# Kernel tuning notes

Measured on AMD Instinct MI355X. Metric: run time of the kernel, lower is better.

The kernel has to match this reference:

```python
import jax, jax.numpy as jnp
import numpy as np

L1, L2, L3, COUNT, B = 3072, 15, 32, 8, 16384

def setup_inputs() -> dict:
    key = jax.random.key(0)
    ks = jax.random.split(key, 10)
    s = 1.0 / np.sqrt(L1)
    inp = {
        'x': jax.random.normal(ks[0], (B, L1), dtype=jnp.float32),
        'ls_indices': jax.random.randint(ks[1], (B,), 0, COUNT, dtype=jnp.int64 if jax.config.jax_enable_x64 else jnp.int32),
        # l1: Linear(L1, (L2+1)*count)
        'l1_w': jax.random.uniform(ks[2], ((L2 + 1) * COUNT, L1), jnp.float32, -s, s),
        'l1_b': jax.random.uniform(ks[3], ((L2 + 1) * COUNT,), jnp.float32, -s, s),
        # l1_fact: Linear(L1, L2+1) -- zero-initialized in the original module
        'l1f_w': jnp.zeros((L2 + 1, L1), jnp.float32),
        'l1f_b': jnp.zeros((L2 + 1,), jnp.float32),
        # l2: Linear(2*L2, L3*count)
        'l2_w': jax.random.uniform(ks[4], (L3 * COUNT, 2 * L2), jnp.float32, -0.18, 0.18),
        'l2_b': jax.random.uniform(ks[5], (L3 * COUNT,), jnp.float32, -0.18, 0.18),
        # output: Linear(L3, count) -- bias zero-initialized
        'out_w': jax.random.uniform(ks[6], (COUNT, L3), jnp.float32, -0.176, 0.176),
        'out_b': jnp.zeros((COUNT,), jnp.float32),
    }
    return inp

def reference(x, ls_indices, l1_w, l1_b, l1f_w, l1f_b, l2_w, l2_b, out_w, out_b):
    Bn = x.shape[0]
    rows = jnp.arange(Bn)
    idx = ls_indices.astype(jnp.int32)

    # l1: compute all stacks, gather selected
    l1s = (x @ l1_w.T + l1_b).reshape(Bn, COUNT, L2 + 1)   # [B, count, 16]
    l1c = l1s[rows, idx]                                    # [B, 16]
    l1f = x @ l1f_w.T + l1f_b                               # [B, 16]
    l1c_main, l1c_out = l1c[:, :L2], l1c[:, L2:]            # [B,15],[B,1]
    l1f_main, l1f_out = l1f[:, :L2], l1f[:, L2:]

    l1x = l1c_main + l1f_main                               # [B, 15]
    l1x = jnp.clip(jnp.concatenate([jnp.square(l1x) * (127.0 / 128.0), l1x], axis=1), 0.0, 1.0)  # [B, 30]

    # l2
    l2s = (l1x @ l2_w.T + l2_b).reshape(Bn, COUNT, L3)      # [B, count, 32]
    l2x = jnp.clip(l2s[rows, idx], 0.0, 1.0)                # [B, 32]

    # output
    l3s = l2x @ out_w.T + out_b                             # [B, count]
    l3c = l3s[rows, idx][:, None]                           # [B, 1]
    return l3c + l1f_out + l1c_out                          # [B, 1]
```

## Files before the change

kernel.cpp:

```cpp
#include <hip/hip_runtime.h>
#include <hip/hip_bf16.h>

#define BATCH 16384
#define K1DIM 3072
#define NCOUNT 8
#define NO 16
#define CHUNK 256
#define NCHUNK (K1DIM / CHUNK)

typedef float f32x4 __attribute__((ext_vector_type(4)));
typedef unsigned int u32;

__host__ __device__ constexpr int brev5(int i) {
    int r = 0;
    for (int b = 0; b < 5; ++b) r |= ((i >> b) & 1) << (4 - b);
    return r;
}

__global__ __launch_bounds__(256) void k_combine(const float* __restrict__ l1w,
                                                 const float* __restrict__ l1fw,
                                                 float* __restrict__ wc) {
    int i = blockIdx.x * 256 + threadIdx.x;
    int row = i / 768;
    int col = (i - row * 768) * 4;
    int o = row & 15;
    f32x4 a = *(const f32x4*)(l1w + (size_t)row * K1DIM + col);
    f32x4 f = *(const f32x4*)(l1fw + (size_t)o * K1DIM + col);
    *(f32x4*)(wc + (size_t)row * K1DIM + col) = a + f;
}

__global__ __launch_bounds__(256) void k_bucket(const int* __restrict__ ls,
                                                int* __restrict__ counts,
                                                int* __restrict__ bucketArr) {
    __shared__ int h[NCOUNT];
    __shared__ int hbase[NCOUNT];
    int t = threadIdx.x;
    if (t < NCOUNT) h[t] = 0;
    __syncthreads();
    int i = blockIdx.x * 256 + t;
    int idx = ls[i];
    int lpos = atomicAdd(&h[idx], 1);
    __syncthreads();
    if (t < NCOUNT) hbase[t] = atomicAdd(&counts[t], h[t]);
    __syncthreads();
    bucketArr[idx * BATCH + hbase[idx] + lpos] = i;
}

__device__ __forceinline__ void stage4(const float* gbase, float* lds_linear,
                                       int wid, int lane) {
#pragma unroll
    for (int i = 0; i < 4; ++i) {
        int row = wid * 4 + i;
        const float* g = gbase + (size_t)row * K1DIM + lane * 4;
        float* l = lds_linear + row * CHUNK;
        __builtin_amdgcn_global_load_lds(
            (const __attribute__((address_space(1))) u32*)g,
            (__attribute__((address_space(3))) u32*)l, 16, 0, 0);
    }
}

__global__ __launch_bounds__(256, 5) void k_gemm(
    const float* __restrict__ x, const float* __restrict__ wc_all,
    const float* __restrict__ l1b, const float* __restrict__ l1fb,
    const int* __restrict__ bucketArr, const int* __restrict__ counts,
    float* __restrict__ y) {
    __shared__ float buf[2][NO * CHUNK];

    int cnt[NCOUNT], off[NCOUNT];
    int nblk = 0;
#pragma unroll
    for (int i = 0; i < NCOUNT; ++i) {
        cnt[i] = counts[i];
        off[i] = nblk;
        nblk += (cnt[i] + 7) >> 3;
    }
    int b = blockIdx.x;
    if (b >= nblk) return;
    int bucket = 0;
#pragma unroll
    for (int i = 1; i < NCOUNT; ++i) if (b >= off[i]) bucket = i;
    int chunkblk = b - off[bucket];
    int count = cnt[bucket];

    int t = threadIdx.x;
    int lane = t & 63;
    int wid = t >> 6;

    const int* bk = bucketArr + bucket * BATCH;
    int base = chunkblk * 8 + wid * 2;
    int g0 = min(base + 0, count - 1);
    int g1 = min(base + 1, count - 1);
    int sid0 = bk[g0], sid1 = bk[g1];
    const float* xr0 = x + (size_t)sid0 * K1DIM + lane * 4;
    const float* xr1 = x + (size_t)sid1 * K1DIM + lane * 4;
    const float* wstack = wc_all + (size_t)bucket * NO * K1DIM;

    float acc[32];
#pragma unroll
    for (int i = 0; i < 32; ++i) acc[i] = 0.f;

    stage4(wstack, &buf[0][0], wid, lane);

    for (int it = 0; it < NCHUNK; ++it) {
        int cur = it & 1;
        __syncthreads();
        if (it + 1 < NCHUNK)
            stage4(wstack + (it + 1) * CHUNK, &buf[cur ^ 1][0], wid, lane);
        int k = it * CHUNK;
        f32x4 xv0 = __builtin_nontemporal_load((const f32x4*)(xr0 + k));
        f32x4 xv1 = __builtin_nontemporal_load((const f32x4*)(xr1 + k));
        const float* lb = &buf[cur][lane * 4];
#pragma unroll
        for (int o = 0; o < NO; ++o) {
            f32x4 wv = *(const f32x4*)(lb + o * CHUNK);
            {
                float& a_ = acc[brev5(o)];
                a_ = fmaf(xv0.x, wv.x, a_);
                a_ = fmaf(xv0.y, wv.y, a_);
                a_ = fmaf(xv0.z, wv.z, a_);
                a_ = fmaf(xv0.w, wv.w, a_);
            }
            {
                float& a_ = acc[brev5(16 + o)];
                a_ = fmaf(xv1.x, wv.x, a_);
                a_ = fmaf(xv1.y, wv.y, a_);
                a_ = fmaf(xv1.z, wv.z, a_);
                a_ = fmaf(xv1.w, wv.w, a_);
            }
        }
    }

#pragma unroll
    for (int i = 0; i < 32; ++i) acc[i] += __shfl_xor(acc[i], 32, 64);
#pragma unroll
    for (int st = 0; st < 5; ++st) {
        const int m = 1 << st;
        const int half = 16 >> st;
        const bool hi = (lane & m) != 0;
#pragma unroll
        for (int i = 0; i < half; ++i) {
            float mine = hi ? acc[i] : acc[i + half];
            float other = __shfl_xor(mine, m, 64);
            float keep = hi ? acc[i + half] : acc[i];
            acc[i] = keep + other;
        }
    }

    if (lane < 32) {
        int p_s = lane >> 4;
        int p_o = lane & 15;
        int gp = min(base + p_s, count - 1);
        int sid = bk[gp];
        float bias = l1b[bucket * NO + p_o] + l1fb[p_o];
        y[(size_t)sid * NO + p_o] = acc[0] + bias;
    }
}

__global__ __launch_bounds__(256) void k_tail(
    const float* __restrict__ y, const int* __restrict__ ls,
    const float* __restrict__ l2w, const float* __restrict__ l2b,
    const float* __restrict__ outw, const float* __restrict__ outb,
    float* __restrict__ out) {
    int gt = blockIdx.x * 256 + threadIdx.x;
    int s = gt >> 5;
    int o2 = gt & 31;
    int idx = ls[s];
    const f32x4* yp = (const f32x4*)(y + (size_t)s * NO);
    f32x4 a0 = yp[0], a1 = yp[1], a2 = yp[2], a3 = yp[3];
    float v[16] = {a0.x, a0.y, a0.z, a0.w, a1.x, a1.y, a1.z, a1.w,
                   a2.x, a2.y, a2.z, a2.w, a3.x, a3.y, a3.z, a3.w};
    float l1x[30];
#pragma unroll
    for (int j = 0; j < 15; ++j) {
        float tv = v[j];
        float sq = tv * tv * (127.f / 128.f);
        l1x[j] = fminf(fmaxf(sq, 0.f), 1.f);
        l1x[j + 15] = fminf(fmaxf(tv, 0.f), 1.f);
    }
    const float* wr = l2w + (size_t)idx * 32 * 30 + o2 * 30;
    float tacc = l2b[idx * 32 + o2];
#pragma unroll
    for (int j = 0; j < 15; ++j) {
        float2 wpv = *(const float2*)(wr + j * 2);
        tacc = fmaf(l1x[j * 2], wpv.x, tacc);
        tacc = fmaf(l1x[j * 2 + 1], wpv.y, tacc);
    }
    tacc = fminf(fmaxf(tacc, 0.f), 1.f);
    float r = tacc * outw[idx * 32 + o2];
#pragma unroll
    for (int m = 1; m < 32; m <<= 1) r += __shfl_xor(r, m, 64);
    if (o2 == 0) out[s] = r + outb[idx] + v[15];
}

extern "C" void kernel_launch(void* const* d_in, const int* in_sizes, int n_in,
                              void* d_out, int out_size, void* d_ws, size_t ws_size,
                              hipStream_t stream) {
    const float* x    = (const float*)d_in[0];
    const int*   ls   = (const int*)  d_in[1];
    const float* l1w  = (const float*)d_in[2];
    const float* l1b  = (const float*)d_in[3];
    const float* l1fw = (const float*)d_in[4];
    const float* l1fb = (const float*)d_in[5];
    const float* l2w  = (const float*)d_in[6];
    const float* l2b  = (const float*)d_in[7];
    const float* outw = (const float*)d_in[8];
    const float* outb = (const float*)d_in[9];
    float* out = (float*)d_out;

    char* ws = (char*)d_ws;
    float* wc       = (float*)ws;
    float* y        = (float*)(ws + 1572864);
    int*   bucketArr= (int*)(ws + 1572864 + 1048576);
    int*   counts   = (int*)(ws + 1572864 + 1048576 + 524288);

    (void)hipMemsetAsync(counts, 0, 32, stream);
    k_combine<<<384, 256, 0, stream>>>(l1w, l1fw, wc);
    k_bucket<<<BATCH / 256, 256, 0, stream>>>(ls, counts, bucketArr);
    k_gemm<<<2055, 256, 0, stream>>>(x, wc, l1b, l1fb, bucketArr, counts, y);
    k_tail<<<BATCH * 32 / 256, 256, 0, stream>>>(y, ls, l2w, l2b, outw, outb, out);
}
```

Baseline: 351.9 us.

## Process eight samples per wave in grouped GEMM to raise weight reuse

Each wave now accumulates 8 samples instead of 2 (32 per block), so every LDS weight vector read serves four times as many FMAs. The split-K reduction is restructured into two 64-accumulator butterflies, and the grid shrinks to 519 blocks with occupancy hint lowered to 2. The x loads also change from nontemporal to normal loads. The cost is many more registers and lower occupancy, which can hurt latency hiding on a kernel that is mostly streaming x.

New measurement: 329.0 us. 6.5% less time.

```diff
diff --git a/kernel.cpp b/kernel.cpp
--- a/kernel.cpp
+++ b/kernel.cpp
@@ -7,13 +7,14 @@
 #define NO 16
 #define CHUNK 256
 #define NCHUNK (K1DIM / CHUNK)
+#define SPB 32
 
 typedef float f32x4 __attribute__((ext_vector_type(4)));
 typedef unsigned int u32;
 
-__host__ __device__ constexpr int brev5(int i) {
+__host__ __device__ constexpr int brev6(int i) {
     int r = 0;
-    for (int b = 0; b < 5; ++b) r |= ((i >> b) & 1) << (4 - b);
+    for (int b = 0; b < 6; ++b) r |= ((i >> b) & 1) << (5 - b);
     return r;
 }
 
@@ -59,7 +60,7 @@
     }
 }
 
-__global__ __launch_bounds__(256, 5) void k_gemm(
+__global__ __launch_bounds__(256, 2) void k_gemm(
     const float* __restrict__ x, const float* __restrict__ wc_all,
     const float* __restrict__ l1b, const float* __restrict__ l1fb,
     const int* __restrict__ bucketArr, const int* __restrict__ counts,
@@ -72,7 +73,7 @@
     for (int i = 0; i < NCOUNT; ++i) {
         cnt[i] = counts[i];
         off[i] = nblk;
-        nblk += (cnt[i] + 7) >> 3;
+        nblk += (cnt[i] + SPB - 1) / SPB;
     }
     int b = blockIdx.x;
     if (b >= nblk) return;
@@ -87,17 +88,18 @@
     int wid = t >> 6;
 
     const int* bk = bucketArr + bucket * BATCH;
-    int base = chunkblk * 8 + wid * 2;
-    int g0 = min(base + 0, count - 1);
-    int g1 = min(base + 1, count - 1);
-    int sid0 = bk[g0], sid1 = bk[g1];
-    const float* xr0 = x + (size_t)sid0 * K1DIM + lane * 4;
-    const float* xr1 = x + (size_t)sid1 * K1DIM + lane * 4;
+    int base = chunkblk * SPB + wid * 8;
+    const float* xr[8];
+#pragma unroll
+    for (int j = 0; j < 8; ++j) {
+        int g = min(base + j, count - 1);
+        xr[j] = x + (size_t)bk[g] * K1DIM + lane * 4;
+    }
     const float* wstack = wc_all + (size_t)bucket * NO * K1DIM;
 
-    float acc[32];
-#pragma unroll
-    for (int i = 0; i < 32; ++i) acc[i] = 0.f;
+    float acc0[64], acc1[64];
+#pragma unroll
+    for (int i = 0; i < 64; ++i) { acc0[i] = 0.f; acc1[i] = 0.f; }
 
     stage4(wstack, &buf[0][0], wid, lane);
 
@@ -107,52 +109,55 @@
         if (it + 1 < NCHUNK)
             stage4(wstack + (it + 1) * CHUNK, &buf[cur ^ 1][0], wid, lane);
         int k = it * CHUNK;
-        f32x4 xv0 = __builtin_nontemporal_load((const f32x4*)(xr0 + k));
-        f32x4 xv1 = __builtin_nontemporal_load((const f32x4*)(xr1 + k));
+        f32x4 xv[8];
+#pragma unroll
+        for (int j = 0; j < 8; ++j) xv[j] = *(const f32x4*)(xr[j] + k);
         const float* lb = &buf[cur][lane * 4];
 #pragma unroll
         for (int o = 0; o < NO; ++o) {
             f32x4 wv = *(const f32x4*)(lb + o * CHUNK);
-            {
-                float& a_ = acc[brev5(o)];
-                a_ = fmaf(xv0.x, wv.x, a_);
-                a_ = fmaf(xv0.y, wv.y, a_);
-                a_ = fmaf(xv0.z, wv.z, a_);
-                a_ = fmaf(xv0.w, wv.w, a_);
+#define ACCUM(A, S, J)                                                   \
+            {                                                            \
+                float& a_ = A[brev6((S)*16 + o)];                        \
+                a_ = fmaf(xv[J].x, wv.x, a_);                            \
+                a_ = fmaf(xv[J].y, wv.y, a_);                            \
+                a_ = fmaf(xv[J].z, wv.z, a_);                            \
+                a_ = fmaf(xv[J].w, wv.w, a_);                            \
             }
-            {
-                float& a_ = acc[brev5(16 + o)];
-                a_ = fmaf(xv1.x, wv.x, a_);
-                a_ = fmaf(xv1.y, wv.y, a_);
-                a_ = fmaf(xv1.z, wv.z, a_);
-                a_ = fmaf(xv1.w, wv.w, a_);
-            }
+            ACCUM(acc0, 0, 0) ACCUM(acc0, 1, 1) ACCUM(acc0, 2, 2) ACCUM(acc0, 3, 3)
+            ACCUM(acc1, 0, 4) ACCUM(acc1, 1, 5) ACCUM(acc1, 2, 6) ACCUM(acc1, 3, 7)
+#undef ACCUM
         }
     }
 
 #pragma unroll
-    for (int i = 0; i < 32; ++i) acc[i] += __shfl_xor(acc[i], 32, 64);
-#pragma unroll
-    for (int st = 0; st < 5; ++st) {
+    for (int st = 0; st < 6; ++st) {
         const int m = 1 << st;
-        const int half = 16 >> st;
+        const int half = 32 >> st;
         const bool hi = (lane & m) != 0;
 #pragma unroll
         for (int i = 0; i < half; ++i) {
-            float mine = hi ? acc[i] : acc[i + half];
+            float mine = hi ? acc0[i] : acc0[i + half];
             float other = __shfl_xor(mine, m, 64);
-            float keep = hi ? acc[i + half] : acc[i];
-            acc[i] = keep + other;
+            float keep = hi ? acc0[i + half] : acc0[i];
+            acc0[i] = keep + other;
+            float mine1 = hi ? acc1[i] : acc1[i + half];
+            float other1 = __shfl_xor(mine1, m, 64);
+            float keep1 = hi ? acc1[i + half] : acc1[i];
+            acc1[i] = keep1 + other1;
         }
     }
 
-    if (lane < 32) {
-        int p_s = lane >> 4;
-        int p_o = lane & 15;
+    int p_s = lane >> 4;
+    int p_o = lane & 15;
+    float bias = l1b[bucket * NO + p_o] + l1fb[p_o];
+    {
         int gp = min(base + p_s, count - 1);
-        int sid = bk[gp];
-        float bias = l1b[bucket * NO + p_o] + l1fb[p_o];
-        y[(size_t)sid * NO + p_o] = acc[0] + bias;
+        y[(size_t)bk[gp] * NO + p_o] = acc0[0] + bias;
+    }
+    {
+        int gp = min(base + 4 + p_s, count - 1);
+        y[(size_t)bk[gp] * NO + p_o] = acc1[0] + bias;
     }
 }
 
@@ -216,6 +221,6 @@
     (void)hipMemsetAsync(counts, 0, 32, stream);
     k_combine<<<384, 256, 0, stream>>>(l1w, l1fw, wc);
     k_bucket<<<BATCH / 256, 256, 0, stream>>>(ls, counts, bucketArr);
-    k_gemm<<<2055, 256, 0, stream>>>(x, wc, l1b, l1fb, bucketArr, counts, y);
+    k_gemm<<<519, 256, 0, stream>>>(x, wc, l1b, l1fb, bucketArr, counts, y);
     k_tail<<<BATCH * 32 / 256, 256, 0, stream>>>(y, ls, l2w, l2b, outw, outb, out);
 }
```
